# Performance work log

Hardware: AMD Instinct MI355X
Metric: run time of the kernel (lower is better)

Reference implementation:

```python
import jax, jax.numpy as jnp
import numpy as np

N_NODES = 100000
N_EDGES = 1600000
IN_DIM = 29
OUT_DIM = 64
BN_EPS = 1e-5


def setup_inputs() -> dict:
    key = jax.random.key(0)
    k1, k2, k3, k4, k5, k6, k7, k8 = jax.random.split(key, 8)
    node = jax.random.normal(k1, (N_NODES, 3), dtype=jnp.float32)
    features = jax.random.normal(k2, (N_NODES, IN_DIM), dtype=jnp.float32)
    edges = jax.random.randint(k3, (N_EDGES, 2), 0, N_NODES, dtype=jnp.int64)
    # Linear(input_dim+3, output_dim, bias=False): weight [out, in+3]
    fan_in = IN_DIM + 3
    weight = jax.random.uniform(k4, (OUT_DIM, fan_in), dtype=jnp.float32,
                                minval=-1.0, maxval=1.0) / np.sqrt(fan_in)
    # BatchNorm1d(output_dim) in eval mode: affine params + running stats
    gamma = jax.random.normal(k5, (OUT_DIM,), dtype=jnp.float32) * 0.1 + 1.0
    beta = jax.random.normal(k6, (OUT_DIM,), dtype=jnp.float32) * 0.1
    running_mean = jax.random.normal(k7, (OUT_DIM,), dtype=jnp.float32) * 0.1
    running_var = jax.random.uniform(k8, (OUT_DIM,), dtype=jnp.float32,
                                     minval=0.5, maxval=1.5)
    return {"node": node, "features": features, "edges": edges,
            "weight": weight, "gamma": gamma, "beta": beta,
            "running_mean": running_mean, "running_var": running_var}


def reference(node, features, edges, weight, gamma, beta, running_mean, running_var):
    dst = edges[:, 0]  # pos_i index (pooling destination)
    src = edges[:, 1]  # pos_j / x_j index
    # gather + concat: msg [E, in+3]
    msg = jnp.concatenate([features[src], node[src] - node[dst]], axis=1)
    # Linear (no bias): [E, out]
    msg = jnp.einsum('ei,oi->eo', msg, weight)
    # BatchNorm1d (eval mode, running stats)
    inv_std = gamma / jnp.sqrt(running_var + BN_EPS)
    msg = (msg - running_mean) * inv_std + beta
    # scatter-max pooling over destination nodes (fixed N segments;
    # torch.unique + scatter_reduce(amax) == segment_max restricted to covered
    # nodes; empty segments filled with 0 matching the zeros init)
    pooled = jax.ops.segment_max(msg, dst, num_segments=N_NODES)
    return jnp.where(jnp.isneginf(pooled), 0.0, pooled)
```

## Files before the change

### kernel.cpp

```cpp
#include <hip/hip_runtime.h>
#include <hip/hip_fp16.h>

#define IN_DIM 29
#define XDIM 32
#define OUT_DIM 64
#define BN_EPS 1e-5f

#define BW      32
#define BW_LOG  5
#define TNODES  64
#define MAXBUCK 4096
#define SENT    0


__global__ __launch_bounds__(256) void fused_tc_kernel(
    const float* __restrict__ features, const float* __restrict__ node,
    const float* __restrict__ weight, const float* __restrict__ gamma,
    const float* __restrict__ rvar, unsigned short* __restrict__ yq,
    const int* __restrict__ edges, int* __restrict__ gHist,
    int n_nodes, int n_edges, int nbuck, int chunk, int nblk)
{
    __shared__ __align__(16) int smem[MAXBUCK];
    if ((int)blockIdx.x < nblk) {
        int* h = smem;
        for (int i = threadIdx.x; i < nbuck; i += 256) h[i] = 0;
        __syncthreads();
        const int e0 = blockIdx.x * chunk;
        const int e1 = min(e0 + chunk, n_edges);
        const int np = (e1 - e0) >> 1;
        const int4* ep4 = (const int4*)(edges + 2 * e0);
        for (int p = threadIdx.x; p < np; p += 256) {
            int4 v = ep4[p];
            atomicAdd(&h[v.x >> BW_LOG], 1);
            atomicAdd(&h[v.z >> BW_LOG], 1);
        }
        if (((e1 - e0) & 1) && threadIdx.x == 0)
            atomicAdd(&h[edges[2 * (e1 - 1)] >> BW_LOG], 1);
        __syncthreads();
        for (int i = threadIdx.x; i < nbuck; i += 256)
            gHist[i * nblk + blockIdx.x] = h[i];
    } else {
        float* stage = (float*)smem;
        const int tid  = threadIdx.x;
        const int lane = tid & 63, wid = tid >> 6;
        const int n0   = ((int)blockIdx.x - nblk) * TNODES;
        const int nrem = min(TNODES, n_nodes - n0);

        for (int idx = tid; idx < nrem * XDIM; idx += 256) {
            const int r = idx >> 5, c = idx & 31;
            float v = (c < IN_DIM) ? features[(size_t)(n0 + r) * IN_DIM + c]
                                   : node[(size_t)(n0 + r) * 3 + (c - IN_DIM)];
            stage[idx] = v;
        }

        const float a = gamma[lane] * __frsqrt_rn(rvar[lane] + BN_EPS);
        float w[XDIM];
        const float4* wp = (const float4*)(weight + lane * XDIM);
#pragma unroll
        for (int q = 0; q < 8; ++q) {
            float4 v = wp[q];
            w[4*q+0] = v.x * a; w[4*q+1] = v.y * a;
            w[4*q+2] = v.z * a; w[4*q+3] = v.w * a;
        }
        __syncthreads();

        const int r0 = wid * (TNODES / 4);
        const int r1 = min(r0 + TNODES / 4, nrem);
        for (int r = r0; r < r1; ++r) {
            const float4* xs = (const float4*)(stage + r * XDIM);
            float a0 = 0.f, a1 = 0.f, a2 = 0.f, a3 = 0.f;
#pragma unroll
            for (int q = 0; q < 8; ++q) {
                float4 x = xs[q];
                a0 = fmaf(x.x, w[4*q+0], a0);
                a1 = fmaf(x.y, w[4*q+1], a1);
                a2 = fmaf(x.z, w[4*q+2], a2);
                a3 = fmaf(x.w, w[4*q+3], a3);
            }
            const float acc = (a0 + a1) + (a2 + a3);
            unsigned short hh = __half_as_ushort(__float2half(acc));
            unsigned short enc = (hh & 0x8000) ? (unsigned short)(~hh)
                                               : (unsigned short)(hh | 0x8000);
            yq[(size_t)(n0 + r) * OUT_DIM + lane] = enc;
        }
    }
}

__global__ __launch_bounds__(256) void scan_a_kernel(
    int* __restrict__ data, int n, int* __restrict__ aux)
{
    const int t = threadIdx.x;
    const int base = blockIdx.x * 1024 + t * 4;
    int v[4];
#pragma unroll
    for (int k = 0; k < 4; ++k) v[k] = (base + k < n) ? data[base + k] : 0;
    int tsum = v[0] + v[1] + v[2] + v[3];

    const int lane = t & 63, wv = t >> 6;
    int x = tsum;
#pragma unroll
    for (int off = 1; off < 64; off <<= 1) {
        int y = __shfl_up(x, off);
        if (lane >= off) x += y;
    }
    __shared__ int wsum[4];
    if (lane == 63) wsum[wv] = x;
    __syncthreads();
    int wexcl = 0;
    for (int i = 0; i < wv; ++i) wexcl += wsum[i];
    int run = wexcl + x - tsum;
#pragma unroll
    for (int k = 0; k < 4; ++k) {
        if (base + k < n) data[base + k] = run;
        run += v[k];
    }
    if (t == 255) aux[blockIdx.x] = run;
}

__global__ __launch_bounds__(256) void scan_b_kernel(int* __restrict__ aux, int nb) {
    const int t = threadIdx.x;
    const int lane = t & 63, wv = t >> 6;
    __shared__ int wsum[4];
    __shared__ int s_run;
    if (t == 0) s_run = 0;
    __syncthreads();
    for (int base = 0; base < nb; base += 256) {
        const int i = base + t;
        int v = (i < nb) ? aux[i] : 0;
        int x = v;
#pragma unroll
        for (int off = 1; off < 64; off <<= 1) {
            int y = __shfl_up(x, off);
            if (lane >= off) x += y;
        }
        if (lane == 63) wsum[wv] = x;
        __syncthreads();
        int wexcl = 0;
        for (int k = 0; k < wv; ++k) wexcl += wsum[k];
        const int run = s_run;
        if (i < nb) aux[i] = run + wexcl + x - v;
        __syncthreads();
        if (t == 255) s_run = run + wexcl + x;
        __syncthreads();
    }
}

__global__ __launch_bounds__(512) void partition_kernel(
    const int* __restrict__ edges, const int* __restrict__ gOffs,
    const int* __restrict__ aux,
    int* __restrict__ keys, int n_edges, int nbuck, int chunk, int nblk)
{
    __shared__ int cur[MAXBUCK];
    for (int i = threadIdx.x; i < nbuck; i += 512) {
        const int idx = i * nblk + blockIdx.x;
        cur[i] = gOffs[idx] + aux[idx >> 10];
    }
    __syncthreads();
    const int e0 = blockIdx.x * chunk;
    const int e1 = min(e0 + chunk, n_edges);
    const int np = (e1 - e0) >> 1;
    const int4* ep4 = (const int4*)(edges + 2 * e0);
    for (int p = threadIdx.x; p < np; p += 512) {
        int4 v = ep4[p];
        const int b0 = v.x >> BW_LOG;
        const int p0 = atomicAdd(&cur[b0], 1);
        keys[p0] = (v.x & (BW - 1)) | (v.y << BW_LOG);
        const int b1 = v.z >> BW_LOG;
        const int p1 = atomicAdd(&cur[b1], 1);
        keys[p1] = (v.z & (BW - 1)) | (v.w << BW_LOG);
    }
    if (((e1 - e0) & 1) && threadIdx.x == 0) {
        const int dst = edges[2 * (e1 - 1)], src = edges[2 * (e1 - 1) + 1];
        const int b = dst >> BW_LOG;
        const int pos = atomicAdd(&cur[b], 1);
        keys[pos] = (dst & (BW - 1)) | (src << BW_LOG);
    }
}

#define LOADQ(V, D, BASE)                                                     \
    _Pragma("unroll")                                                         \
    for (int u = 0; u < 16; ++u) {                                            \
        const int key = __builtin_amdgcn_readlane(kv, (BASE) + u);            \
        D[u] = key & (BW - 1);                                                \
        V[u] = yq[(size_t)((unsigned)key >> BW_LOG) * OUT_DIM + lane];        \
    }

#define ATOMQ(V, D)                                                           \
    _Pragma("unroll")                                                         \
    for (int u = 0; u < 16; ++u)                                              \
        atomicMax(&acc[D[u] * OUT_DIM + lane], (int)V[u]);

__global__ __launch_bounds__(512, 4) void pool_fused_kernel(
    const int* __restrict__ gOffs, const int* __restrict__ aux,
    const int* __restrict__ keys,
    const unsigned short* __restrict__ yq, const float* __restrict__ node,
    const float* __restrict__ weight, const float* __restrict__ gamma,
    const float* __restrict__ beta, const float* __restrict__ rmean,
    const float* __restrict__ rvar,
    float* __restrict__ out, int n_nodes, int n_edges, int nbuck, int nblk)
{
    __shared__ int acc[BW * OUT_DIM];
    const int tid = threadIdx.x;
    const int lane = tid & 63, wid = tid >> 6;
    const int b = blockIdx.x;

    {
        int4* p = (int4*)acc;
        for (int i = tid; i < BW * OUT_DIM / 4; i += 512)
            p[i] = make_int4(SENT, SENT, SENT, SENT);
    }
    __syncthreads();

    const int i0 = b * nblk;
    const int beg = gOffs[i0] + aux[i0 >> 10];
    int end;
    if (b == nbuck - 1) end = n_edges;
    else {
        const int i1 = (b + 1) * nblk;
        end = gOffs[i1] + aux[i1 >> 10];
    }

    const int cnt = end - beg;
    const int slice = (cnt + 7) >> 3;
    const int w_beg = beg + wid * slice;
    const int w_end = min(w_beg + slice, end);

    if (w_beg < w_end) {
        const int last = w_end - 1;
        int j = w_beg;
        int kv = keys[min(j + lane, last)];
        while (j < w_end) {
            const int jn = j + 64;
            int kv_n = 0;
            if (jn < w_end) kv_n = keys[min(jn + lane, last)];

            unsigned int va[16]; int da[16];
            unsigned int vb[16]; int db[16];
            LOADQ(va, da, 0)
            LOADQ(vb, db, 16)
            ATOMQ(va, da)
            LOADQ(va, da, 32)
            ATOMQ(vb, db)
            LOADQ(vb, db, 48)
            ATOMQ(va, da)
            ATOMQ(vb, db)

            j = jn; kv = kv_n;
        }
    }
    __syncthreads();

    const float a  = gamma[lane] * __frsqrt_rn(rvar[lane] + BN_EPS);
    const float bp = beta[lane] - rmean[lane] * a;
    const float w29 = weight[lane * XDIM + 29] * a;
    const float w30 = weight[lane * XDIM + 30] * a;
    const float w31 = weight[lane * XDIM + 31] * a;

    for (int d = wid; d < BW; d += 8) {
        const int dg = b * BW + d;
        if (dg >= n_nodes) break;
        const int k = acc[d * OUT_DIM + lane];
        float rr;
        if (k == SENT) {
            rr = 0.0f;
        } else {
            const unsigned short enc = (unsigned short)k;
            const unsigned short h = (enc & 0x8000) ? (unsigned short)(enc ^ 0x8000)
                                                    : (unsigned short)(~enc);
            const float v = __half2float(__ushort_as_half(h));
            const float nx = node[(size_t)dg * 3 + 0];
            const float ny = node[(size_t)dg * 3 + 1];
            const float nz = node[(size_t)dg * 3 + 2];
            rr = v + (bp - (w29 * nx + w30 * ny + w31 * nz));
        }
        out[(size_t)dg * OUT_DIM + lane] = rr;
    }
}

__global__ void init_kernel(int4* __restrict__ out, int total4) {
    int t = blockIdx.x * blockDim.x + threadIdx.x;
    if (t < total4) out[t] = make_int4(INT_MIN, INT_MIN, INT_MIN, INT_MIN);
}

__global__ __launch_bounds__(256) void edge_atomic_kernel(
    const int* __restrict__ edges,
    const float* __restrict__ features, const float* __restrict__ node,
    const float* __restrict__ weight, const float* __restrict__ gamma,
    const float* __restrict__ beta, const float* __restrict__ rmean,
    const float* __restrict__ rvar,
    int* __restrict__ out, int n_edges, int epw)
{
    const int lane = threadIdx.x & 63;
    const int wave = (blockIdx.x * blockDim.x + threadIdx.x) >> 6;
    int e0 = wave * epw, e1 = e0 + epw;
    if (e1 > n_edges) e1 = n_edges;

    float w[XDIM];
    const float4* wp = (const float4*)(weight + lane * XDIM);
#pragma unroll
    for (int q = 0; q < 8; ++q) {
        float4 v = wp[q];
        w[4*q+0] = v.x; w[4*q+1] = v.y; w[4*q+2] = v.z; w[4*q+3] = v.w;
    }
    const float a = gamma[lane] * __frsqrt_rn(rvar[lane] + BN_EPS);
    const float bprime = beta[lane] - rmean[lane] * a;

    for (int e = e0; e < e1; ++e) {
        const int dst = edges[2*e+0], src = edges[2*e+1];
        float x[XDIM];
#pragma unroll
        for (int i = 0; i < IN_DIM; ++i) x[i] = features[(size_t)src * IN_DIM + i];
#pragma unroll
        for (int j = 0; j < 3; ++j)
            x[IN_DIM+j] = node[(size_t)src*3+j] - node[(size_t)dst*3+j];
        float acc = 0.0f;
#pragma unroll
        for (int i = 0; i < XDIM; ++i) acc = fmaf(x[i], w[i], acc);
        float msg = fmaf(acc, a, bprime);
        int bb = __float_as_int(msg);
        int key = (bb < 0) ? (bb ^ 0x7FFFFFFF) : bb;
        atomicMax(out + (size_t)dst * OUT_DIM + lane, key);
    }
}

__global__ void decode_kernel(int* __restrict__ out, int total) {
    int t = blockIdx.x * blockDim.x + threadIdx.x;
    if (t >= total) return;
    int k = out[t];
    float r;
    if (k == INT_MIN) r = 0.0f;
    else { int b = (k < 0) ? (k ^ 0x7FFFFFFF) : k; r = __int_as_float(b); }
    ((float*)out)[t] = r;
}

extern "C" void kernel_launch(void* const* d_in, const int* in_sizes, int n_in,
                              void* d_out, int out_size, void* d_ws, size_t ws_size,
                              hipStream_t stream) {
    const float* node     = (const float*)d_in[0];
    const float* features = (const float*)d_in[1];
    const int*   edges    = (const int*)d_in[2];
    const float* weight   = (const float*)d_in[3];
    const float* gamma    = (const float*)d_in[4];
    const float* beta     = (const float*)d_in[5];
    const float* rmean    = (const float*)d_in[6];
    const float* rvar     = (const float*)d_in[7];

    const int n_nodes = in_sizes[0] / 3;
    const int n_edges = in_sizes[2] / 2;

    const int nbuck = (n_nodes + BW - 1) >> BW_LOG;

    int nblk = 0; size_t o_yq=0, o_hist=0, o_aux=0, o_keys=0; size_t need = 0;
    for (int cand = 256; cand >= 32; cand >>= 1) {
        const int n_scan = nbuck * cand;
        const int nb_scan = (n_scan + 1023) / 1024;
        size_t off = 0;
        auto alloc = [&](size_t bytes) { size_t r = off; off = (off + bytes + 15) & ~(size_t)15; return r; };
        o_yq   = alloc((size_t)n_nodes * OUT_DIM * sizeof(unsigned short));
        o_hist = alloc((size_t)n_scan * sizeof(int));
        o_aux  = alloc((size_t)nb_scan * sizeof(int));
        o_keys = alloc((size_t)n_edges * sizeof(int));
        need = off;
        if (need <= ws_size) { nblk = cand; break; }
    }

    if (nblk > 0 && nbuck <= MAXBUCK && n_nodes <= MAXBUCK * BW) {
        const int n_scan = nbuck * nblk;
        const int nb_scan = (n_scan + 1023) / 1024;
        int chunk = (n_edges + nblk - 1) / nblk;
        chunk = (chunk + 1) & ~1;
        const int ntb = (n_nodes + TNODES - 1) / TNODES;

        char* base  = (char*)d_ws;
        unsigned short* yq = (unsigned short*)(base + o_yq);
        int* gHist  = (int*)(base + o_hist);
        int* aux    = (int*)(base + o_aux);
        int* keys   = (int*)(base + o_keys);

        fused_tc_kernel<<<nblk + ntb, 256, 0, stream>>>(
            features, node, weight, gamma, rvar, yq,
            edges, gHist, n_nodes, n_edges, nbuck, chunk, nblk);
        scan_a_kernel<<<nb_scan, 256, 0, stream>>>(gHist, n_scan, aux);
        scan_b_kernel<<<1, 256, 0, stream>>>(aux, nb_scan);
        partition_kernel<<<nblk, 512, 0, stream>>>(edges, gHist, aux, keys,
                                                   n_edges, nbuck, chunk, nblk);
        pool_fused_kernel<<<nbuck, 512, 0, stream>>>(
            gHist, aux, keys, yq, node, weight, gamma, beta, rmean, rvar,
            (float*)d_out, n_nodes, n_edges, nbuck, nblk);
    } else {
        int* out_i = (int*)d_out;
        const int total4 = out_size / 4;
        init_kernel<<<(total4 + 255) / 256, 256, 0, stream>>>((int4*)out_i, total4);
        const int n_waves = 8192;
        const int epw = (n_edges + n_waves - 1) / n_waves;
        edge_atomic_kernel<<<n_waves / 4, 256, 0, stream>>>(
            edges, features, node, weight, gamma, beta, rmean, rvar,
            out_i, n_edges, epw);
        decode_kernel<<<(out_size + 255) / 256, 256, 0, stream>>>(out_i, out_size);
    }
}
```

Before: 189.0 us.

## Fuse histogram, scan and partition into one kernel with block-local key segments

The histogram blocks now do a local exclusive scan and partition their own edge chunk into block-local key segments, writing per-block bucket offsets. This removes the global scan kernels and the separate partition kernel, cutting three launches and the global-offset round trip. The pool kernel gathers each bucket's key pieces from all nblk blocks, stages them in shared memory when they fit, and falls back to a slower serial path otherwise. In exchange it adds scattered reads of many small segments per bucket and more shared memory per pool block, and nblk is capped at 128.

```diff
diff --git a/kernel.cpp b/kernel.cpp
--- a/kernel.cpp
+++ b/kernel.cpp
@@ -10,6 +10,8 @@
 #define BW_LOG  5
 #define TNODES  64
 #define MAXBUCK 4096
+#define MAXNBLK 128
+#define KCAP    4096
 #define SENT    0
 
 
@@ -17,31 +19,71 @@
     const float* __restrict__ features, const float* __restrict__ node,
     const float* __restrict__ weight, const float* __restrict__ gamma,
     const float* __restrict__ rvar, unsigned short* __restrict__ yq,
-    const int* __restrict__ edges, int* __restrict__ gHist,
+    const int* __restrict__ edges, int* __restrict__ offs,
+    int* __restrict__ keys,
     int n_nodes, int n_edges, int nbuck, int chunk, int nblk)
 {
     __shared__ __align__(16) int smem[MAXBUCK];
+    __shared__ int wsum[4];
+    const int tid = threadIdx.x;
     if ((int)blockIdx.x < nblk) {
         int* h = smem;
-        for (int i = threadIdx.x; i < nbuck; i += 256) h[i] = 0;
+        for (int i = tid; i < nbuck; i += 256) h[i] = 0;
         __syncthreads();
         const int e0 = blockIdx.x * chunk;
         const int e1 = min(e0 + chunk, n_edges);
-        const int np = (e1 - e0) >> 1;
+        const int len = (e1 > e0) ? (e1 - e0) : 0;
+        const int np = len >> 1;
         const int4* ep4 = (const int4*)(edges + 2 * e0);
-        for (int p = threadIdx.x; p < np; p += 256) {
+        for (int p = tid; p < np; p += 256) {
             int4 v = ep4[p];
             atomicAdd(&h[v.x >> BW_LOG], 1);
             atomicAdd(&h[v.z >> BW_LOG], 1);
         }
-        if (((e1 - e0) & 1) && threadIdx.x == 0)
+        if ((len & 1) && tid == 0)
             atomicAdd(&h[edges[2 * (e1 - 1)] >> BW_LOG], 1);
         __syncthreads();
-        for (int i = threadIdx.x; i < nbuck; i += 256)
-            gHist[i * nblk + blockIdx.x] = h[i];
+
+        const int SER = (nbuck + 255) / 256;
+        const int lo = tid * SER, hi = min(lo + SER, nbuck);
+        int sum = 0;
+        for (int i = lo; i < hi; ++i) sum += h[i];
+        const int lane = tid & 63, wv = tid >> 6;
+        int x = sum;
+#pragma unroll
+        for (int off = 1; off < 64; off <<= 1) {
+            int y = __shfl_up(x, off);
+            if (lane >= off) x += y;
+        }
+        if (lane == 63) wsum[wv] = x;
+        __syncthreads();
+        int wex = 0;
+        for (int k = 0; k < wv; ++k) wex += wsum[k];
+        int run = wex + x - sum;
+        for (int i = lo; i < hi; ++i) { int t = h[i]; h[i] = run; run += t; }
+        __syncthreads();
+
+        int* orow = offs + (size_t)blockIdx.x * (nbuck + 1);
+        for (int i = tid; i < nbuck; i += 256) orow[i] = h[i];
+        if (tid == 0) orow[nbuck] = len;
+        __syncthreads();
+
+        for (int p = tid; p < np; p += 256) {
+            int4 v = ep4[p];
+            const int b0 = v.x >> BW_LOG;
+            const int p0 = atomicAdd(&h[b0], 1);
+            keys[e0 + p0] = (v.x & (BW - 1)) | (v.y << BW_LOG);
+            const int b1 = v.z >> BW_LOG;
+            const int p1 = atomicAdd(&h[b1], 1);
+            keys[e0 + p1] = (v.z & (BW - 1)) | (v.w << BW_LOG);
+        }
+        if ((len & 1) && tid == 0) {
+            const int dst = edges[2 * (e1 - 1)], src = edges[2 * (e1 - 1) + 1];
+            const int pos = atomicAdd(&h[dst >> BW_LOG], 1);
+            keys[e0 + pos] = (dst & (BW - 1)) | (src << BW_LOG);
+        }
     } else {
         float* stage = (float*)smem;
-        const int tid  = threadIdx.x;
         const int lane = tid & 63, wid = tid >> 6;
         const int n0   = ((int)blockIdx.x - nblk) * TNODES;
         const int nrem = min(TNODES, n_nodes - n0);
@@ -71,11 +113,11 @@
             float a0 = 0.f, a1 = 0.f, a2 = 0.f, a3 = 0.f;
 #pragma unroll
             for (int q = 0; q < 8; ++q) {
-                float4 x = xs[q];
-                a0 = fmaf(x.x, w[4*q+0], a0);
-                a1 = fmaf(x.y, w[4*q+1], a1);
-                a2 = fmaf(x.z, w[4*q+2], a2);
-                a3 = fmaf(x.w, w[4*q+3], a3);
+                float4 x4 = xs[q];
+                a0 = fmaf(x4.x, w[4*q+0], a0);
+                a1 = fmaf(x4.y, w[4*q+1], a1);
+                a2 = fmaf(x4.z, w[4*q+2], a2);
+                a3 = fmaf(x4.w, w[4*q+3], a3);
             }
             const float acc = (a0 + a1) + (a2 + a3);
             unsigned short hh = __half_as_ushort(__float2half(acc));
@@ -86,97 +128,6 @@
     }
 }
 
-__global__ __launch_bounds__(256) void scan_a_kernel(
-    int* __restrict__ data, int n, int* __restrict__ aux)
-{
-    const int t = threadIdx.x;
-    const int base = blockIdx.x * 1024 + t * 4;
-    int v[4];
-#pragma unroll
-    for (int k = 0; k < 4; ++k) v[k] = (base + k < n) ? data[base + k] : 0;
-    int tsum = v[0] + v[1] + v[2] + v[3];
-
-    const int lane = t & 63, wv = t >> 6;
-    int x = tsum;
-#pragma unroll
-    for (int off = 1; off < 64; off <<= 1) {
-        int y = __shfl_up(x, off);
-        if (lane >= off) x += y;
-    }
-    __shared__ int wsum[4];
-    if (lane == 63) wsum[wv] = x;
-    __syncthreads();
-    int wexcl = 0;
-    for (int i = 0; i < wv; ++i) wexcl += wsum[i];
-    int run = wexcl + x - tsum;
-#pragma unroll
-    for (int k = 0; k < 4; ++k) {
-        if (base + k < n) data[base + k] = run;
-        run += v[k];
-    }
-    if (t == 255) aux[blockIdx.x] = run;
-}
-
-__global__ __launch_bounds__(256) void scan_b_kernel(int* __restrict__ aux, int nb) {
-    const int t = threadIdx.x;
-    const int lane = t & 63, wv = t >> 6;
-    __shared__ int wsum[4];
-    __shared__ int s_run;
-    if (t == 0) s_run = 0;
-    __syncthreads();
-    for (int base = 0; base < nb; base += 256) {
-        const int i = base + t;
-        int v = (i < nb) ? aux[i] : 0;
-        int x = v;
-#pragma unroll
-        for (int off = 1; off < 64; off <<= 1) {
-            int y = __shfl_up(x, off);
-            if (lane >= off) x += y;
-        }
-        if (lane == 63) wsum[wv] = x;
-        __syncthreads();
-        int wexcl = 0;
-        for (int k = 0; k < wv; ++k) wexcl += wsum[k];
-        const int run = s_run;
-        if (i < nb) aux[i] = run + wexcl + x - v;
-        __syncthreads();
-        if (t == 255) s_run = run + wexcl + x;
-        __syncthreads();
-    }
-}
-
-__global__ __launch_bounds__(512) void partition_kernel(
-    const int* __restrict__ edges, const int* __restrict__ gOffs,
-    const int* __restrict__ aux,
-    int* __restrict__ keys, int n_edges, int nbuck, int chunk, int nblk)
-{
-    __shared__ int cur[MAXBUCK];
-    for (int i = threadIdx.x; i < nbuck; i += 512) {
-        const int idx = i * nblk + blockIdx.x;
-        cur[i] = gOffs[idx] + aux[idx >> 10];
-    }
-    __syncthreads();
-    const int e0 = blockIdx.x * chunk;
-    const int e1 = min(e0 + chunk, n_edges);
-    const int np = (e1 - e0) >> 1;
-    const int4* ep4 = (const int4*)(edges + 2 * e0);
-    for (int p = threadIdx.x; p < np; p += 512) {
-        int4 v = ep4[p];
-        const int b0 = v.x >> BW_LOG;
-        const int p0 = atomicAdd(&cur[b0], 1);
-        keys[p0] = (v.x & (BW - 1)) | (v.y << BW_LOG);
-        const int b1 = v.z >> BW_LOG;
-        const int p1 = atomicAdd(&cur[b1], 1);
-        keys[p1] = (v.z & (BW - 1)) | (v.w << BW_LOG);
-    }
-    if (((e1 - e0) & 1) && threadIdx.x == 0) {
-        const int dst = edges[2 * (e1 - 1)], src = edges[2 * (e1 - 1) + 1];
-        const int b = dst >> BW_LOG;
-        const int pos = atomicAdd(&cur[b], 1);
-        keys[pos] = (dst & (BW - 1)) | (src << BW_LOG);
-    }
-}
-
 #define LOADQ(V, D, BASE)                                                     \
     _Pragma("unroll")                                                         \
     for (int u = 0; u < 16; ++u) {                                            \
@@ -191,15 +142,17 @@
         atomicMax(&acc[D[u] * OUT_DIM + lane], (int)V[u]);
 
 __global__ __launch_bounds__(512, 4) void pool_fused_kernel(
-    const int* __restrict__ gOffs, const int* __restrict__ aux,
-    const int* __restrict__ keys,
+    const int* __restrict__ offs, const int* __restrict__ keys,
     const unsigned short* __restrict__ yq, const float* __restrict__ node,
     const float* __restrict__ weight, const float* __restrict__ gamma,
     const float* __restrict__ beta, const float* __restrict__ rmean,
     const float* __restrict__ rvar,
-    float* __restrict__ out, int n_nodes, int n_edges, int nbuck, int nblk)
+    float* __restrict__ out, int n_nodes, int nbuck, int chunk, int nblk)
 {
+    __shared__ int skeys[KCAP];
     __shared__ int acc[BW * OUT_DIM];
+    __shared__ int sstart[MAXNBLK];
+    __shared__ int spref[MAXNBLK + 1];
     const int tid = threadIdx.x;
     const int lane = tid & 63, wid = tid >> 6;
     const int b = blockIdx.x;
@@ -209,43 +162,86 @@
         for (int i = tid; i < BW * OUT_DIM / 4; i += 512)
             p[i] = make_int4(SENT, SENT, SENT, SENT);
     }
+
+    if (tid < nblk) {
+        const int* orow = offs + (size_t)tid * (nbuck + 1) + b;
+        const int s = orow[0];
+        const int e = orow[1];
+        sstart[tid] = tid * chunk + s;
+        spref[tid]  = e - s;
+    }
     __syncthreads();
 
-    const int i0 = b * nblk;
-    const int beg = gOffs[i0] + aux[i0 >> 10];
-    int end;
-    if (b == nbuck - 1) end = n_edges;
-    else {
-        const int i1 = (b + 1) * nblk;
-        end = gOffs[i1] + aux[i1 >> 10];
-    }
-
-    const int cnt = end - beg;
-    const int slice = (cnt + 7) >> 3;
-    const int w_beg = beg + wid * slice;
-    const int w_end = min(w_beg + slice, end);
-
-    if (w_beg < w_end) {
-        const int last = w_end - 1;
-        int j = w_beg;
-        int kv = keys[min(j + lane, last)];
-        while (j < w_end) {
-            const int jn = j + 64;
-            int kv_n = 0;
-            if (jn < w_end) kv_n = keys[min(jn + lane, last)];
-
-            unsigned int va[16]; int da[16];
-            unsigned int vb[16]; int db[16];
-            LOADQ(va, da, 0)
-            LOADQ(vb, db, 16)
-            ATOMQ(va, da)
-            LOADQ(va, da, 32)
-            ATOMQ(vb, db)
-            LOADQ(vb, db, 48)
-            ATOMQ(va, da)
-            ATOMQ(vb, db)
-
-            j = jn; kv = kv_n;
+    if (wid == 0) {
+        int c0 = (lane < nblk) ? spref[lane] : 0;
+        int x0 = c0;
+#pragma unroll
+        for (int off = 1; off < 64; off <<= 1) {
+            int y = __shfl_up(x0, off);
+            if (lane >= off) x0 += y;
+        }
+        const int tot0 = __shfl(x0, 63);
+        int c1 = (64 + lane < nblk) ? spref[64 + lane] : 0;
+        int x1 = c1;
+#pragma unroll
+        for (int off = 1; off < 64; off <<= 1) {
+            int y = __shfl_up(x1, off);
+            if (lane >= off) x1 += y;
+        }
+        const int tot1 = __shfl(x1, 63);
+        if (lane < nblk) spref[lane] = x0 - c0;
+        if (64 + lane < nblk) spref[64 + lane] = tot0 + x1 - c1;
+        if (lane == 0) spref[nblk] = tot0 + tot1;
+    }
+    __syncthreads();
+    const int cnt = spref[nblk];
+
+    if (cnt <= KCAP) {
+        for (int k = wid; k < nblk; k += 8) {
+            const int bg = sstart[k];
+            const int bs = spref[k];
+            const int ck = spref[k + 1] - bs;
+            for (int j = lane; j < ck; j += 64)
+                skeys[bs + j] = keys[bg + j];
+        }
+        __syncthreads();
+
+        const int slice = (cnt + 7) >> 3;
+        const int w_beg = wid * slice;
+        const int w_end = min(w_beg + slice, cnt);
+        if (w_beg < w_end) {
+            const int last = w_end - 1;
+            int j = w_beg;
+            int kv = skeys[min(j + lane, last)];
+            while (j < w_end) {
+                const int jn = j + 64;
+                int kv_n = 0;
+                if (jn < w_end) kv_n = skeys[min(jn + lane, last)];
+
+                unsigned int va[16]; int da[16];
+                unsigned int vb[16]; int db[16];
+                LOADQ(va, da, 0)
+                LOADQ(vb, db, 16)
+                ATOMQ(va, da)
+                LOADQ(va, da, 32)
+                ATOMQ(vb, db)
+                LOADQ(vb, db, 48)
+                ATOMQ(va, da)
+                ATOMQ(vb, db)
+
+                j = jn; kv = kv_n;
+            }
+        }
+    } else {
+        for (int k = wid; k < nblk; k += 8) {
+            const int bg = sstart[k];
+            const int ck = spref[k + 1] - spref[k];
+            for (int j = 0; j < ck; ++j) {
+                const int key = keys[bg + j];
+                const int d = key & (BW - 1);
+                const unsigned int v = yq[(size_t)((unsigned)key >> BW_LOG) * OUT_DIM + lane];
+                atomicMax(&acc[d * OUT_DIM + lane], (int)v);
+            }
         }
     }
     __syncthreads();
@@ -350,43 +346,33 @@
 
     const int nbuck = (n_nodes + BW - 1) >> BW_LOG;
 
-    int nblk = 0; size_t o_yq=0, o_hist=0, o_aux=0, o_keys=0; size_t need = 0;
-    for (int cand = 256; cand >= 32; cand >>= 1) {
-        const int n_scan = nbuck * cand;
-        const int nb_scan = (n_scan + 1023) / 1024;
+    int nblk = 0; size_t o_yq=0, o_offs=0, o_keys=0; size_t need = 0;
+    for (int cand = MAXNBLK; cand >= 32; cand >>= 1) {
         size_t off = 0;
         auto alloc = [&](size_t bytes) { size_t r = off; off = (off + bytes + 15) & ~(size_t)15; return r; };
         o_yq   = alloc((size_t)n_nodes * OUT_DIM * sizeof(unsigned short));
-        o_hist = alloc((size_t)n_scan * sizeof(int));
-        o_aux  = alloc((size_t)nb_scan * sizeof(int));
+        o_offs = alloc((size_t)cand * (nbuck + 1) * sizeof(int));
         o_keys = alloc((size_t)n_edges * sizeof(int));
         need = off;
         if (need <= ws_size) { nblk = cand; break; }
     }
 
     if (nblk > 0 && nbuck <= MAXBUCK && n_nodes <= MAXBUCK * BW) {
-        const int n_scan = nbuck * nblk;
-        const int nb_scan = (n_scan + 1023) / 1024;
         int chunk = (n_edges + nblk - 1) / nblk;
         chunk = (chunk + 1) & ~1;
         const int ntb = (n_nodes + TNODES - 1) / TNODES;
 
         char* base  = (char*)d_ws;
         unsigned short* yq = (unsigned short*)(base + o_yq);
-        int* gHist  = (int*)(base + o_hist);
-        int* aux    = (int*)(base + o_aux);
+        int* offs   = (int*)(base + o_offs);
         int* keys   = (int*)(base + o_keys);
 
         fused_tc_kernel<<<nblk + ntb, 256, 0, stream>>>(
             features, node, weight, gamma, rvar, yq,
-            edges, gHist, n_nodes, n_edges, nbuck, chunk, nblk);
-        scan_a_kernel<<<nb_scan, 256, 0, stream>>>(gHist, n_scan, aux);
-        scan_b_kernel<<<1, 256, 0, stream>>>(aux, nb_scan);
-        partition_kernel<<<nblk, 512, 0, stream>>>(edges, gHist, aux, keys,
-                                                   n_edges, nbuck, chunk, nblk);
+            edges, offs, keys, n_nodes, n_edges, nbuck, chunk, nblk);
         pool_fused_kernel<<<nbuck, 512, 0, stream>>>(
-            gHist, aux, keys, yq, node, weight, gamma, beta, rmean, rvar,
-            (float*)d_out, n_nodes, n_edges, nbuck, nblk);
+            offs, keys, yq, node, weight, gamma, beta, rmean, rvar,
+            (float*)d_out, n_nodes, nbuck, chunk, nblk);
     } else {
         int* out_i = (int*)d_out;
         const int total4 = out_size / 4;
```

Result: no change. 189.7 us (+0.4%).
